# Kernel tuning notes

Hardware: AMD Instinct MI355X
Metric: run time of the kernel (lower is better)

The kernel has to match this reference:

```python
import math
import jax, jax.numpy as jnp
import numpy as np

B, L, H, E = 2, 2048, 8, 64
S, D = 2048, 64


def _row_mask(index, sub_len, win_len, log_l):
    # Faithful to torch code, including the swapped-arg call convention:
    # called with sub_len = L (query len), win_len = S (key len).
    mask = np.zeros(win_len, dtype=np.float32)
    if (win_len // sub_len) * 2 * log_l > index:
        mask[: index + 1] = 1.0
    else:
        while index >= 0:
            if index - log_l + 1 < 0:
                mask[:index] = 1.0
                break
            mask[index - log_l + 1 : index + 1] = 1.0
            for i in range(log_l):
                new_index = index - log_l + 1 - 2 ** i
                if index - new_index <= sub_len and new_index >= 0:
                    mask[new_index] = 1.0
            index -= sub_len
    return mask


def _log_mask(win_len, sub_len):
    # mirrors LogSparseAttention.log_mask(L, S) with its swapped row_mask call
    log_l = math.ceil(np.log2(win_len))  # log2 of query length L
    m = np.zeros((win_len, sub_len), dtype=np.float32)
    for i in range(win_len):
        m[i] = _row_mask(i, win_len, sub_len, log_l)
    return jnp.asarray(m)[None, None]  # [1,1,L,S]


_MASK = _log_mask(L, S)


def setup_inputs() -> dict:
    key = jax.random.key(0)
    kq, kk, kv = jax.random.split(key, 3)
    return {
        "queries": jax.random.normal(kq, (B, L, H, E), dtype=jnp.float32),
        "keys": jax.random.normal(kk, (B, S, H, E), dtype=jnp.float32),
        "values": jax.random.normal(kv, (B, S, H, D), dtype=jnp.float32),
        "attention_mask": jnp.ones((1,), dtype=bool),  # unused, as in the torch module
    }


def reference(queries, keys, values, attention_mask):
    scale = 1.0 / math.sqrt(queries.shape[-1])
    scores = jnp.einsum("blhe,bshe->bhls", queries, keys)  # [B,H,L,S]
    mask = _MASK[:, :, : scores.shape[-2], : scores.shape[-1]]
    scores = scores * mask + (-1e9) * (1.0 - mask)
    A = jax.nn.softmax(scale * scores, axis=-1)  # dropout = identity in eval
    V = jnp.einsum("bhls,bshd->blhd", A, values)  # [B,L,H,D]
    return V
```

## Files before the change

kernel.cpp:

```cpp
#include <hip/hip_runtime.h>


#define BB 2
#define LL 2048
#define HH 8
#define EE 64
#define SS 2048

__device__ __forceinline__ unsigned short bf16_rne(float f) {
    unsigned int u = __float_as_uint(f);
    unsigned int r = u + 0x7FFFu + ((u >> 16) & 1u);
    return (unsigned short)(r >> 16);
}

template<int CTRL>
__device__ __forceinline__ float dpp_add(float v) {
    int t = __builtin_amdgcn_mov_dpp(__float_as_int(v), CTRL, 0xF, 0xF, false);
    return v + __int_as_float(t);
}

__device__ __forceinline__ void unpack8(const uint4 kv, float* e) {
    e[0] = __int_as_float((int)(kv.x << 16));
    e[1] = __int_as_float((int)(kv.x & 0xFFFF0000u));
    e[2] = __int_as_float((int)(kv.y << 16));
    e[3] = __int_as_float((int)(kv.y & 0xFFFF0000u));
    e[4] = __int_as_float((int)(kv.z << 16));
    e[5] = __int_as_float((int)(kv.z & 0xFFFF0000u));
    e[6] = __int_as_float((int)(kv.w << 16));
    e[7] = __int_as_float((int)(kv.w & 0xFFFF0000u));
}

__global__ __launch_bounds__(256) void pack_kv_kernel(
    const float* __restrict__ K, const float* __restrict__ V,
    unsigned short* __restrict__ P)
{
    const int j = blockIdx.x * 256 + threadIdx.x;
    const int p = j & 7;
    const int h = (j >> 3) & (HH - 1);
    const int s = (j >> 6) & (SS - 1);
    const int b = j >> 17;
    const size_t src = (((size_t)b * SS + s) * HH + h) * EE + 8 * p;
    const float4 k0 = *(const float4*)(K + src);
    const float4 k1 = *(const float4*)(K + src + 4);
    const float4 v0 = *(const float4*)(V + src);
    const float4 v1 = *(const float4*)(V + src + 4);
    uint4 kw, vw;
    kw.x = bf16_rne(k0.x) | ((unsigned)bf16_rne(k0.y) << 16);
    kw.y = bf16_rne(k0.z) | ((unsigned)bf16_rne(k0.w) << 16);
    kw.z = bf16_rne(k1.x) | ((unsigned)bf16_rne(k1.y) << 16);
    kw.w = bf16_rne(k1.z) | ((unsigned)bf16_rne(k1.w) << 16);
    vw.x = bf16_rne(v0.x) | ((unsigned)bf16_rne(v0.y) << 16);
    vw.y = bf16_rne(v0.z) | ((unsigned)bf16_rne(v0.w) << 16);
    vw.z = bf16_rne(v1.x) | ((unsigned)bf16_rne(v1.y) << 16);
    vw.w = bf16_rne(v1.z) | ((unsigned)bf16_rne(v1.w) << 16);
    const size_t n = ((size_t)b * HH + h) * SS + s;
    *(uint4*)(P + n * 128 + 8 * p)      = kw;
    *(uint4*)(P + n * 128 + 64 + 8 * p) = vw;
}

__global__ __launch_bounds__(256) void logsparse_attn_kernel(
    const float* __restrict__ Q,
    const unsigned short* __restrict__ P,
    float* __restrict__ O)
{
    const int lane = threadIdx.x & 63;
    const int wv   = threadIdx.x >> 6;
    const int lb  = ((blockIdx.x & 7) << 10) | (blockIdx.x >> 3);
    const int row = lb * 4 + wv;
    const int l  = row % LL;
    const int bh = row / LL;

    const int t  = lane & 15;
    const int g  = lane >> 4;
    const int t8 = t & 7;

    const size_t qbase = ((size_t)(bh / HH) * LL + l) * HH * EE + (size_t)(bh & (HH - 1)) * EE;
    float qr[8];
    {
        const float4 a  = *(const float4*)(Q + qbase + 8 * t8);
        const float4 b4 = *(const float4*)(Q + qbase + 8 * t8 + 4);
        qr[0] = a.x;  qr[1] = a.y;  qr[2] = a.z;  qr[3] = a.w;
        qr[4] = b4.x; qr[5] = b4.y; qr[6] = b4.z; qr[7] = b4.w;
    }

    const unsigned short* Pbh = P + (size_t)bh * SS * 128;

    int ntaps, nkeys, w0;
    if (l < 22) { ntaps = 0; nkeys = l + 1; w0 = 0; }
    else {
        w0 = l - 10;
        ntaps = 32 - __clz(w0);
        if (ntaps > 11) ntaps = 11;
        nkeys = ntaps + 11;
    }

    uint4 kv[6];
    #pragma unroll
    for (int c = 0; c < 6; ++c) {
        const int n  = 4 * c + g;
        const int nc = (n < nkeys) ? n : (nkeys - 1);
        int key;
        if (l < 22)           key = nc;
        else if (nc < ntaps)  key = w0 - (1 << (ntaps - 1 - nc));
        else                  key = w0 + (nc - ntaps);
        kv[c] = *(const uint4*)(Pbh + ((size_t)key << 7) + 8 * t);
    }

    float sc[6];
    #pragma unroll
    for (int c = 0; c < 6; ++c) {
        float e[8];
        unpack8(kv[c], e);
        float p = qr[0]*e[0] + qr[1]*e[1] + qr[2]*e[2] + qr[3]*e[3]
                + qr[4]*e[4] + qr[5]*e[5] + qr[6]*e[6] + qr[7]*e[7];
        p = (t < 8) ? p : 0.0f;
        p = dpp_add<0xB1>(p);
        p = dpp_add<0x4E>(p);
        p = dpp_add<0x124>(p);
        p = dpp_add<0x128>(p);
        sc[c] = ((4 * c + g) < nkeys) ? p * 0.125f : -1e30f;
    }

    float mg = sc[0];
    #pragma unroll
    for (int c = 1; c < 6; ++c) mg = fmaxf(mg, sc[c]);

    float lsum = 0.0f;
    float acc[8] = {0.f,0.f,0.f,0.f,0.f,0.f,0.f,0.f};
    #pragma unroll
    for (int c = 0; c < 6; ++c) {
        const float w = __expf(sc[c] - mg);
        lsum += w;
        float e[8];
        unpack8(kv[c], e);
        #pragma unroll
        for (int j = 0; j < 8; ++j) acc[j] += w * e[j];
    }

    float M = mg;
    M = fmaxf(M, __shfl_xor(M, 16, 64));
    M = fmaxf(M, __shfl_xor(M, 32, 64));
    const float r = __expf(mg - M);
    lsum *= r;
    #pragma unroll
    for (int j = 0; j < 8; ++j) acc[j] *= r;

    lsum += __shfl_xor(lsum, 16, 64);
    lsum += __shfl_xor(lsum, 32, 64);
    #pragma unroll
    for (int j = 0; j < 8; ++j) {
        acc[j] += __shfl_xor(acc[j], 16, 64);
        acc[j] += __shfl_xor(acc[j], 32, 64);
    }

    if (g == 0 && t >= 8) {
        const float inv = 1.0f / lsum;
        float4 o0, o1;
        o0.x = acc[0]*inv; o0.y = acc[1]*inv; o0.z = acc[2]*inv; o0.w = acc[3]*inv;
        o1.x = acc[4]*inv; o1.y = acc[5]*inv; o1.z = acc[6]*inv; o1.w = acc[7]*inv;
        *(float4*)(O + qbase + 8 * t8)     = o0;
        *(float4*)(O + qbase + 8 * t8 + 4) = o1;
    }
}

extern "C" void kernel_launch(void* const* d_in, const int* in_sizes, int n_in,
                              void* d_out, int out_size, void* d_ws, size_t ws_size,
                              hipStream_t stream) {
    const float* Q = (const float*)d_in[0];
    const float* K = (const float*)d_in[1];
    const float* V = (const float*)d_in[2];
    float* O = (float*)d_out;
    unsigned short* P = (unsigned short*)d_ws;

    hipLaunchKernelGGL(pack_kv_kernel, dim3((BB*SS*HH*8)/256), dim3(256), 0, stream,
                       K, V, P);
    hipLaunchKernelGGL(logsparse_attn_kernel, dim3((BB*HH*LL)/4), dim3(256), 0, stream,
                       Q, P, O);
}
```

Baseline: 94.44 us.

## Fuse KV bf16 packing into attention kernel via shared-memory key window staging

Removes the separate pack kernel and its global workspace round trip. Each 1024-thread block now handles 16 consecutive query rows of one (b,h) and stages the union of keys they need (local window plus the log-spaced taps) into shared memory as bf16. Queries then gather their keys from LDS slots instead of global memory. This saves one launch and the global write and re-read of packed K/V. In exchange, taps shared between neighbouring blocks are converted more than once, and the slot arithmetic is tricky to get right.

New measurement: 97.53 us. 3.3% more time.

```diff
diff --git a/kernel.cpp b/kernel.cpp
--- a/kernel.cpp
+++ b/kernel.cpp
@@ -6,6 +6,8 @@
 #define HH 8
 #define EE 64
 #define SS 2048
+#define TROWS 16
+#define NSLOT 138
 
 __device__ __forceinline__ unsigned short bf16_rne(float f) {
     unsigned int u = __float_as_uint(f);
@@ -30,51 +32,53 @@
     e[7] = __int_as_float((int)(kv.w & 0xFFFF0000u));
 }
 
-__global__ __launch_bounds__(256) void pack_kv_kernel(
-    const float* __restrict__ K, const float* __restrict__ V,
-    unsigned short* __restrict__ P)
-{
-    const int j = blockIdx.x * 256 + threadIdx.x;
-    const int p = j & 7;
-    const int h = (j >> 3) & (HH - 1);
-    const int s = (j >> 6) & (SS - 1);
-    const int b = j >> 17;
-    const size_t src = (((size_t)b * SS + s) * HH + h) * EE + 8 * p;
-    const float4 k0 = *(const float4*)(K + src);
-    const float4 k1 = *(const float4*)(K + src + 4);
-    const float4 v0 = *(const float4*)(V + src);
-    const float4 v1 = *(const float4*)(V + src + 4);
-    uint4 kw, vw;
-    kw.x = bf16_rne(k0.x) | ((unsigned)bf16_rne(k0.y) << 16);
-    kw.y = bf16_rne(k0.z) | ((unsigned)bf16_rne(k0.w) << 16);
-    kw.z = bf16_rne(k1.x) | ((unsigned)bf16_rne(k1.y) << 16);
-    kw.w = bf16_rne(k1.z) | ((unsigned)bf16_rne(k1.w) << 16);
-    vw.x = bf16_rne(v0.x) | ((unsigned)bf16_rne(v0.y) << 16);
-    vw.y = bf16_rne(v0.z) | ((unsigned)bf16_rne(v0.w) << 16);
-    vw.z = bf16_rne(v1.x) | ((unsigned)bf16_rne(v1.y) << 16);
-    vw.w = bf16_rne(v1.z) | ((unsigned)bf16_rne(v1.w) << 16);
-    const size_t n = ((size_t)b * HH + h) * SS + s;
-    *(uint4*)(P + n * 128 + 8 * p)      = kw;
-    *(uint4*)(P + n * 128 + 64 + 8 * p) = vw;
-}
-
-__global__ __launch_bounds__(256) void logsparse_attn_kernel(
+__global__ __launch_bounds__(1024, 4) void logsparse_attn_kernel(
     const float* __restrict__ Q,
-    const unsigned short* __restrict__ P,
+    const float* __restrict__ K,
+    const float* __restrict__ V,
     float* __restrict__ O)
 {
-    const int lane = threadIdx.x & 63;
-    const int wv   = threadIdx.x >> 6;
-    const int lb  = ((blockIdx.x & 7) << 10) | (blockIdx.x >> 3);
-    const int row = lb * 4 + wv;
-    const int l  = row % LL;
-    const int bh = row / LL;
+    __shared__ unsigned short smem[NSLOT * 128];
 
-    const int t  = lane & 15;
-    const int g  = lane >> 4;
-    const int t8 = t & 7;
+    const int tid = threadIdx.x;
+    const int lb = ((blockIdx.x & 7) << 8) | (blockIdx.x >> 3);
+    const int bh = lb >> 7;
+    const int l0 = (lb & 127) << 4;
+    const int b  = bh >> 3;
+    const int h  = bh & 7;
 
-    const size_t qbase = ((size_t)(bh / HH) * LL + l) * HH * EE + (size_t)(bh & (HH - 1)) * EE;
+    const size_t bhbase = (size_t)b * SS * HH * EE + (size_t)h * EE;
+    #pragma unroll
+    for (int it = 0; it < 3; ++it) {
+        const int j = it * 1024 + tid;
+        if (j < NSLOT * 16) {
+            const int r = j >> 4;
+            const int p = j & 15;
+            int s = (r < 42) ? (l0 - 26 + r)
+                             : (l0 - 10 - (32 << ((r - 42) >> 4)) + ((r - 42) & 15));
+            s = min(max(s, 0), SS - 1);
+            const float* src = ((p < 8) ? K : V) + bhbase
+                             + (size_t)s * (HH * EE) + ((size_t)(p & 7) << 3);
+            const float4 a = *(const float4*)src;
+            const float4 c = *(const float4*)(src + 4);
+            uint4 w;
+            w.x = bf16_rne(a.x) | ((unsigned)bf16_rne(a.y) << 16);
+            w.y = bf16_rne(a.z) | ((unsigned)bf16_rne(a.w) << 16);
+            w.z = bf16_rne(c.x) | ((unsigned)bf16_rne(c.y) << 16);
+            w.w = bf16_rne(c.z) | ((unsigned)bf16_rne(c.w) << 16);
+            *(uint4*)(smem + r * 128 + p * 8) = w;
+        }
+    }
+    __syncthreads();
+
+    const int lane = tid & 63;
+    const int wv   = tid >> 6;
+    const int l    = l0 + wv;
+    const int t    = lane & 15;
+    const int g    = lane >> 4;
+    const int t8   = t & 7;
+
+    const size_t qbase = ((size_t)b * LL + l) * HH * EE + (size_t)h * EE;
     float qr[8];
     {
         const float4 a  = *(const float4*)(Q + qbase + 8 * t8);
@@ -82,8 +86,6 @@
         qr[0] = a.x;  qr[1] = a.y;  qr[2] = a.z;  qr[3] = a.w;
         qr[4] = b4.x; qr[5] = b4.y; qr[6] = b4.z; qr[7] = b4.w;
     }
-
-    const unsigned short* Pbh = P + (size_t)bh * SS * 128;
 
     int ntaps, nkeys, w0;
     if (l < 22) { ntaps = 0; nkeys = l + 1; w0 = 0; }
@@ -99,11 +101,14 @@
     for (int c = 0; c < 6; ++c) {
         const int n  = 4 * c + g;
         const int nc = (n < nkeys) ? n : (nkeys - 1);
-        int key;
-        if (l < 22)           key = nc;
-        else if (nc < ntaps)  key = w0 - (1 << (ntaps - 1 - nc));
-        else                  key = w0 + (nc - ntaps);
-        kv[c] = *(const uint4*)(Pbh + ((size_t)key << 7) + 8 * t);
+        int slot;
+        if (l < 22) slot = nc + 26 - l0;
+        else if (nc < ntaps) {
+            const int i = ntaps - 1 - nc;
+            slot = (i <= 4) ? ((l - l0) + 16 - (1 << i))
+                            : (42 + ((i - 5) << 4) + (l - l0));
+        } else slot = (w0 + nc - ntaps) - l0 + 26;
+        kv[c] = *(const uint4*)(smem + slot * 128 + t * 8);
     }
 
     float sc[6];
@@ -170,10 +175,8 @@
     const float* K = (const float*)d_in[1];
     const float* V = (const float*)d_in[2];
     float* O = (float*)d_out;
-    unsigned short* P = (unsigned short*)d_ws;
 
-    hipLaunchKernelGGL(pack_kv_kernel, dim3((BB*SS*HH*8)/256), dim3(256), 0, stream,
-                       K, V, P);
-    hipLaunchKernelGGL(logsparse_attn_kernel, dim3((BB*HH*LL)/4), dim3(256), 0, stream,
-                       Q, P, O);
+    const int blocks = (BB * HH * LL) / TROWS;
+    hipLaunchKernelGGL(logsparse_attn_kernel, dim3(blocks), dim3(1024), 0, stream,
+                       Q, K, V, O);
 }
```
